# Kernel tuning notes

Hardware: AMD Instinct MI355X
Metric: run time of the kernel (lower is better)

## Reference

```python
import jax, jax.numpy as jnp
import numpy as np

ALPHA = 0.2  # LeakyReLU slope in GAT
OUT_SLOPE = 0.01  # default nn.LeakyyReLU slope for self.out
B, E, IN_DIM, HID, HEADS = 4, 2048, 32, 18, 3
DH = HID // HEADS  # per-head out dim = 6


def _leaky(x, slope):
    return jnp.where(x > 0, x, slope * x)


def _gat_head(x, adj, W, a):
    # x: [B,E,in], W: [in,dh], a: [2*dh,1]
    h = jnp.einsum('bei,id->bed', x, W)                      # [B,E,dh]
    d = h.shape[-1]
    # score[b,i,j] = leakyrelu(a . concat(h_i, h_j)) = leakyrelu(h_i.a1 + h_j.a2)
    e1 = jnp.einsum('bed,d->be', h, a[:d, 0])
    e2 = jnp.einsum('bed,d->be', h, a[d:, 0])
    score = _leaky(e1[:, :, None] + e2[:, None, :], ALPHA)   # [B,E,E]
    scores = jnp.where(adj == 1.0, score, 0.0)
    logits = jnp.where(adj > 0.0, scores, -30.0)
    att = jax.nn.softmax(logits, axis=2)                     # softmax over j
    # h_prime[b,j,d] = sum_i att[b,i,j] * h[b,i,d]  (torch sums over dim=1)
    h_prime = jnp.einsum('bij,bid->bjd', att, h)
    return jax.nn.elu(h_prime)  # concat=True -> elu


def _gat_multihead(x, adj, Ws, As):
    # Ws: [H,in,dh], As: [H,2*dh,1]
    outs = jax.vmap(lambda W, a: _gat_head(x, adj, W, a))(Ws, As)  # [H,B,E,dh]
    H, b, e, d = outs.shape
    return jnp.moveaxis(outs, 0, 2).reshape(b, e, H * d)  # concat heads last-dim


def _gcn(x, adj2d, W, b):
    return adj2d @ (x @ W) + b


def setup_inputs() -> dict:
    key = jax.random.key(0)
    ks = jax.random.split(key, 16)
    node_input = jax.random.normal(ks[0], (B, E, IN_DIM), jnp.float32)
    uv_filed = jax.random.normal(ks[1], (B, E, IN_DIM), jnp.float32)
    adj = jax.random.randint(ks[2], (B, E, E), 0, 2).astype(jnp.float32)
    s = 0.1
    Wt1 = jax.random.normal(ks[3], (HEADS, IN_DIM, DH), jnp.float32) * s
    at1 = jax.random.normal(ks[4], (HEADS, 2 * DH, 1), jnp.float32) * s
    Wt2 = jax.random.normal(ks[5], (HEADS, IN_DIM, DH), jnp.float32) * s
    at2 = jax.random.normal(ks[6], (HEADS, 2 * DH, 1), jnp.float32) * s
    Wg1 = jax.random.normal(ks[7], (HID, 16), jnp.float32) * s
    bg1 = jnp.zeros((16,), jnp.float32)
    Wg2 = jax.random.normal(ks[8], (16, 2), jnp.float32) * s
    bg2 = jnp.zeros((2,), jnp.float32)
    Wo1 = jax.random.normal(ks[9], (HID, 16), jnp.float32) * s
    bo1 = jnp.zeros((16,), jnp.float32)
    Wo2 = jax.random.normal(ks[10], (16, 2), jnp.float32) * s
    bo2 = jnp.zeros((2,), jnp.float32)
    return dict(node_input=node_input, uv_filed=uv_filed, adj=adj,
                Wt1=Wt1, at1=at1, Wt2=Wt2, at2=at2,
                Wg1=Wg1, bg1=bg1, Wg2=Wg2, bg2=bg2,
                Wo1=Wo1, bo1=bo1, Wo2=Wo2, bo2=bo2)


def reference(node_input, uv_filed, adj, Wt1, at1, Wt2, at2,
              Wg1, bg1, Wg2, bg2, Wo1, bo1, Wo2, bo2):
    h = _gat_multihead(node_input, adj, Wt1, at1)  # [B,E,18]
    o = _gat_multihead(uv_filed, adj, Wt2, at2)    # [B,E,18]
    a0 = adj[0]
    Y = jax.nn.relu(_gcn(h[0], a0, Wg1, bg1))
    O = jax.nn.relu(_gcn(o[0], a0, Wo1, bo1))
    Y = _gcn(Y, a0, Wg2, bg2)
    O = _gcn(O, a0, Wo2, bo2)
    return (jax.nn.log_softmax(Y, axis=1), _leaky(O, OUT_SLOPE))
```

## Files before the change

kernel.cpp:

```cpp
#include <hip/hip_runtime.h>
#include <hip/hip_bf16.h>


__global__ __launch_bounds__(256) void k01(
    const float* __restrict__ adj0, unsigned int* __restrict__ bm,
    const float* __restrict__ node, const float* __restrict__ uv,
    const float* __restrict__ Wt1, const float* __restrict__ at1,
    const float* __restrict__ Wt2, const float* __restrict__ at2,
    float* __restrict__ hcol, float* __restrict__ pack1, float* __restrict__ pack2) {
  int b = blockIdx.x;
  if (b < 512) {
    int lane = threadIdx.x & 63, w = threadIdx.x >> 6;
    int row = b * 4 + w;
    const float* arow = adj0 + (size_t)row * 2048;
#pragma unroll 4
    for (int it = 0; it < 32; ++it) {
      float v = arow[it * 64 + lane];
      unsigned long long mask = __ballot(v == 1.0f);
      if (lane == 0) bm[row * 64 + it * 2] = (unsigned int)mask;
      else if (lane == 32) bm[row * 64 + it * 2 + 1] = (unsigned int)(mask >> 32);
    }
    return;
  }
  __shared__ float sW[192];
  __shared__ float sA[12];
  int fb = b - 512;
  int g = fb / 24;
  int h = (fb / 8) % 3;
  int e = (fb % 8) * 256 + threadIdx.x;
  const float* W = (g ? Wt2 : Wt1) + h * 192;
  const float* A = (g ? at2 : at1) + h * 12;
  const float* x = (g ? uv : node) + e * 32;
  if (threadIdx.x < 192) sW[threadIdx.x] = W[threadIdx.x];
  if (threadIdx.x < 12) sA[threadIdx.x] = A[threadIdx.x];
  __syncthreads();
  float xv[32];
#pragma unroll
  for (int i = 0; i < 32; ++i) xv[i] = x[i];
  float hv[6];
#pragma unroll
  for (int d = 0; d < 6; ++d) hv[d] = 0.f;
#pragma unroll
  for (int i = 0; i < 32; ++i)
#pragma unroll
    for (int d = 0; d < 6; ++d) hv[d] += xv[i] * sW[i * 6 + d];
  float e1 = 0.f, e2 = 0.f;
#pragma unroll
  for (int d = 0; d < 6; ++d) {
    e1 += hv[d] * sA[d];
    e2 += hv[d] * sA[6 + d];
  }
  int c = g * 3 + h;
#pragma unroll
  for (int d = 0; d < 6; ++d) hcol[(c * 6 + d) * 2048 + e] = hv[d];
  pack1[c * 2048 + e] = e1;
  pack1[(6 + c) * 2048 + e] = __expf(e1);
  pack1[(12 + c) * 2048 + e] = __expf(0.2f * e1);
  pack2[c * 2048 + e] = e2;
  pack2[(6 + c) * 2048 + e] = __expf(e2);
  pack2[(12 + c) * 2048 + e] = __expf(0.2f * e2);
}

__global__ __launch_bounds__(384) void k2_rowsum(
    const unsigned int* __restrict__ bm, const float* __restrict__ pack1,
    const float* __restrict__ pack2, float* __restrict__ invrs) {
  int tid = threadIdx.x;
  int c = tid >> 6, lane = tid & 63;
  int i0 = blockIdx.x * 8;
  const float4* p2_4 = (const float4*)pack2;
  float e1r[8], p1r[8], q1r[8], sum[8];
#pragma unroll
  for (int r = 0; r < 8; ++r) {
    e1r[r] = pack1[c * 2048 + i0 + r];
    p1r[r] = pack1[(6 + c) * 2048 + i0 + r];
    q1r[r] = pack1[(12 + c) * 2048 + i0 + r];
    sum[r] = 0.f;
  }
  int sh = (lane & 7) * 4;
#pragma unroll
  for (int it = 0; it < 8; ++it) {
    int j4 = it * 64 + lane;
    float4 e2 = p2_4[c * 512 + j4];
    float4 p2 = p2_4[(6 + c) * 512 + j4];
    float4 q2 = p2_4[(12 + c) * 512 + j4];
    int wbase = it * 8 + (lane >> 3);
    float abx, aby, abz, abw;
#pragma unroll
    for (int r = 0; r < 8; ++r) {
      unsigned int wd = bm[(i0 + r) * 64 + wbase] >> sh;
      { float e = e1r[r] + e2.x; bool p = e > 0.f;
        abx = (p ? p1r[r] : q1r[r]) * (p ? p2.x : q2.x); }
      { float e = e1r[r] + e2.y; bool p = e > 0.f;
        aby = (p ? p1r[r] : q1r[r]) * (p ? p2.y : q2.y); }
      { float e = e1r[r] + e2.z; bool p = e > 0.f;
        abz = (p ? p1r[r] : q1r[r]) * (p ? p2.z : q2.z); }
      { float e = e1r[r] + e2.w; bool p = e > 0.f;
        abw = (p ? p1r[r] : q1r[r]) * (p ? p2.w : q2.w); }
      float s = ((wd & 1u) ? abx : 0.f) + ((wd & 2u) ? aby : 0.f) +
                ((wd & 4u) ? abz : 0.f) + ((wd & 8u) ? abw : 0.f);
      sum[r] += s;
    }
  }
#pragma unroll
  for (int r = 0; r < 8; ++r) {
#pragma unroll
    for (int off = 32; off > 0; off >>= 1) sum[r] += __shfl_down(sum[r], off);
  }
  if (lane == 0) {
#pragma unroll
    for (int r = 0; r < 8; ++r) invrs[c * 2048 + i0 + r] = 1.0f / sum[r];
  }
}

__global__ __launch_bounds__(384) void k3_hprime(
    const unsigned int* __restrict__ bm, const float* __restrict__ hcol,
    const float* __restrict__ pack1, const float* __restrict__ pack2,
    const float* __restrict__ invrs, float* __restrict__ hp_part) {
  __shared__ float4 sPack[6 * 64];
  __shared__ float sHS[6 * 64 * 8];
  __shared__ unsigned int sM[64 * 4];
  float4* sHS4 = (float4*)sHS;
  int tid = threadIdx.x;
  int c6 = tid >> 6, jl = tid & 63;
  int j0 = blockIdx.x * 128;
  int jA = j0 + jl, jB = jA + 64;
  float e2A = pack2[c6 * 2048 + jA];
  float p2A = pack2[(6 + c6) * 2048 + jA];
  float q2A = pack2[(12 + c6) * 2048 + jA];
  float e2B = pack2[c6 * 2048 + jB];
  float p2B = pack2[(6 + c6) * 2048 + jB];
  float q2B = pack2[(12 + c6) * 2048 + jB];
  float aA0 = 0.f, aA1 = 0.f, aA2 = 0.f, aA3 = 0.f, aA4 = 0.f, aA5 = 0.f;
  float aB0 = 0.f, aB1 = 0.f, aB2 = 0.f, aB3 = 0.f, aB4 = 0.f, aB5 = 0.f;
  int hi = jl >> 5;
  int shj = jl & 31;
  int ibeg = blockIdx.y * 128;
  for (int i0 = ibeg; i0 < ibeg + 128; i0 += 64) {
    __syncthreads();
    {
      int cc = c6, ii = jl;
      float e1 = pack1[cc * 2048 + i0 + ii];
      float p1 = pack1[(6 + cc) * 2048 + i0 + ii];
      float q1 = pack1[(12 + cc) * 2048 + i0 + ii];
      sPack[cc * 64 + ii] = make_float4(e1, p1, q1, 0.f);
      float iv = invrs[cc * 2048 + i0 + ii];
#pragma unroll
      for (int d = 0; d < 6; ++d)
        sHS[(cc * 64 + ii) * 8 + d] = hcol[(cc * 6 + d) * 2048 + i0 + ii] * iv;
      sHS[(cc * 64 + ii) * 8 + 6] = 0.f;
      sHS[(cc * 64 + ii) * 8 + 7] = 0.f;
    }
    if (tid < 256) sM[tid] = bm[(size_t)(i0 + (tid >> 2)) * 64 + (j0 >> 5) + (tid & 3)];
    __syncthreads();
#pragma unroll 8
    for (int ii = 0; ii < 64; ++ii) {
      float4 pk = sPack[c6 * 64 + ii];
      float4 h0 = sHS4[(c6 * 64 + ii) * 2];
      float4 h1 = sHS4[(c6 * 64 + ii) * 2 + 1];
      unsigned int wdA = sM[ii * 4 + hi];
      unsigned int wdB = sM[ii * 4 + 2 + hi];
      {
        float e = pk.x + e2A; bool p = e > 0.f;
        float ab = (p ? pk.y : pk.z) * (p ? p2A : q2A);
        float wgt = ((wdA >> shj) & 1u) ? ab : 0.f;
        aA0 += wgt * h0.x; aA1 += wgt * h0.y; aA2 += wgt * h0.z;
        aA3 += wgt * h0.w; aA4 += wgt * h1.x; aA5 += wgt * h1.y;
      }
      {
        float e = pk.x + e2B; bool p = e > 0.f;
        float ab = (p ? pk.y : pk.z) * (p ? p2B : q2B);
        float wgt = ((wdB >> shj) & 1u) ? ab : 0.f;
        aB0 += wgt * h0.x; aB1 += wgt * h0.y; aB2 += wgt * h0.z;
        aB3 += wgt * h0.w; aB4 += wgt * h1.x; aB5 += wgt * h1.y;
      }
    }
  }
  float* hp = hp_part + (size_t)blockIdx.y * 73728;
  int kb = c6 * 6;
  hp[(kb + 0) * 2048 + jA] = aA0;
  hp[(kb + 1) * 2048 + jA] = aA1;
  hp[(kb + 2) * 2048 + jA] = aA2;
  hp[(kb + 3) * 2048 + jA] = aA3;
  hp[(kb + 4) * 2048 + jA] = aA4;
  hp[(kb + 5) * 2048 + jA] = aA5;
  hp[(kb + 0) * 2048 + jB] = aB0;
  hp[(kb + 1) * 2048 + jB] = aB1;
  hp[(kb + 2) * 2048 + jB] = aB2;
  hp[(kb + 3) * 2048 + jB] = aB3;
  hp[(kb + 4) * 2048 + jB] = aB4;
  hp[(kb + 5) * 2048 + jB] = aB5;
}

__global__ __launch_bounds__(256) void k4_T(
    const float* __restrict__ hp_part, const float* __restrict__ Wg1,
    const float* __restrict__ Wo1, float* __restrict__ T) {
  __shared__ float sHP[16 * 37];
  __shared__ float sWg[288], sWo[288];
  int tid = threadIdx.x;
  int j0 = blockIdx.x * 16;
  for (int idx = tid; idx < 288; idx += 256) {
    sWg[idx] = Wg1[idx];
    sWo[idx] = Wo1[idx];
  }
  for (int idx = tid; idx < 576; idx += 256) {
    int r = idx >> 4, jl = idx & 15;
    float s = 0.f;
#pragma unroll
    for (int sp = 0; sp < 16; ++sp)
      s += hp_part[(size_t)sp * 73728 + r * 2048 + j0 + jl];
    sHP[jl * 37 + r] = s;
  }
  __syncthreads();
  int jl = tid & 15, wq = tid >> 4;
  int gat = wq >> 3;
  int c0 = (wq & 7) * 2;
  const float* Wp = gat ? sWo : sWg;
  float a0 = 0.f, a1 = 0.f;
#pragma unroll
  for (int r = 0; r < 18; ++r) {
    float x = sHP[jl * 37 + gat * 18 + r];
    float hc = x > 0.f ? x : __expf(x) - 1.f;
    a0 += hc * Wp[r * 16 + c0];
    a1 += hc * Wp[r * 16 + c0 + 1];
  }
  T[(j0 + jl) * 32 + gat * 16 + c0] = a0;
  T[(j0 + jl) * 32 + gat * 16 + c0 + 1] = a1;
}

__global__ __launch_bounds__(256) void k5_gcn1(
    const unsigned int* __restrict__ bm, const float* __restrict__ T,
    float* __restrict__ Craw_part) {
  __shared__ unsigned int sM[64 * 4];
  __shared__ float4 sT4[128 * 8];
  const float4* T4 = (const float4*)T;
  int tid = threadIdx.x;
  int rl = tid & 31, cg = tid >> 5;
  int i0 = blockIdx.x * 64;
  int k0 = blockIdx.y * 128;
  sM[tid] = bm[(size_t)(i0 + (tid >> 2)) * 64 + (k0 >> 5) + (tid & 3)];
  for (int idx = tid; idx < 1024; idx += 256) sT4[idx] = T4[k0 * 8 + idx];
  __syncthreads();
  float a0x = 0.f, a0y = 0.f, a0z = 0.f, a0w = 0.f;
  float a1x = 0.f, a1y = 0.f, a1z = 0.f, a1w = 0.f;
#pragma unroll
  for (int wi = 0; wi < 4; ++wi) {
    unsigned int wA = sM[rl * 4 + wi];
    unsigned int wB = sM[(rl + 32) * 4 + wi];
#pragma unroll 16
    for (int kb = 0; kb < 32; ++kb) {
      float4 t = sT4[(wi * 32 + kb) * 8 + cg];
      float mA = (float)((wA >> kb) & 1u);
      float mB = (float)((wB >> kb) & 1u);
      a0x += mA * t.x; a0y += mA * t.y; a0z += mA * t.z; a0w += mA * t.w;
      a1x += mB * t.x; a1y += mB * t.y; a1z += mB * t.z; a1w += mB * t.w;
    }
  }
  float* base = Craw_part + (size_t)blockIdx.y * 65536;
  *(float4*)&base[(i0 + rl) * 32 + cg * 4] = make_float4(a0x, a0y, a0z, a0w);
  *(float4*)&base[(i0 + rl + 32) * 32 + cg * 4] = make_float4(a1x, a1y, a1z, a1w);
}

__global__ __launch_bounds__(256) void k6_T2(
    const float* __restrict__ Craw_part, const float* __restrict__ bg1,
    const float* __restrict__ Wg2, const float* __restrict__ bo1,
    const float* __restrict__ Wo2, float* __restrict__ T2) {
  int tid = threadIdx.x;
  int wave = tid >> 6, lane = tid & 63;
  int j = blockIdx.x * 8 + wave * 2 + (lane >> 5);
  int cl = lane & 31;
  int gat = cl >> 4, cc = cl & 15;
  float x = 0.f;
#pragma unroll
  for (int sp = 0; sp < 16; ++sp) x += Craw_part[(size_t)sp * 65536 + j * 32 + cl];
  x += gat ? bo1[cc] : bg1[cc];
  x = x > 0.f ? x : 0.f;
  float wa = gat ? Wo2[cc * 2 + 0] : Wg2[cc * 2 + 0];
  float wb = gat ? Wo2[cc * 2 + 1] : Wg2[cc * 2 + 1];
  float pa = x * wa, pb = x * wb;
#pragma unroll
  for (int m = 8; m > 0; m >>= 1) {
    pa += __shfl_xor(pa, m);
    pb += __shfl_xor(pb, m);
  }
  if (cc == 0) {
    T2[j * 4 + gat * 2 + 0] = pa;
    T2[j * 4 + gat * 2 + 1] = pb;
  }
}

__global__ __launch_bounds__(256) void k7_final(
    const unsigned int* __restrict__ bm, const float* __restrict__ T2,
    const float* __restrict__ bg2, const float* __restrict__ bo2,
    float* __restrict__ out) {
  int tid = threadIdx.x;
  int lane = tid & 63, w = tid >> 6;
  int r = blockIdx.x * 4 + w;
  const float4* T24 = (const float4*)T2;
  float4 acc = make_float4(0.f, 0.f, 0.f, 0.f);
  int sh = lane & 31;
#pragma unroll 8
  for (int it = 0; it < 32; ++it) {
    int k = it * 64 + lane;
    unsigned int wd = bm[r * 64 + it * 2 + (lane >> 5)];
    float m = (float)((wd >> sh) & 1u);
    float4 t = T24[k];
    acc.x += m * t.x;
    acc.y += m * t.y;
    acc.z += m * t.z;
    acc.w += m * t.w;
  }
#pragma unroll
  for (int off = 32; off > 0; off >>= 1) {
    acc.x += __shfl_down(acc.x, off);
    acc.y += __shfl_down(acc.y, off);
    acc.z += __shfl_down(acc.z, off);
    acc.w += __shfl_down(acc.w, off);
  }
  if (lane == 0) {
    float y0 = acc.x + bg2[0], y1 = acc.y + bg2[1];
    float m = fmaxf(y0, y1);
    float ls = m + logf(__expf(y0 - m) + __expf(y1 - m));
    out[r * 2 + 0] = y0 - ls;
    out[r * 2 + 1] = y1 - ls;
    float o0 = acc.z + bo2[0], o1 = acc.w + bo2[1];
    out[4096 + r * 2 + 0] = o0 > 0.f ? o0 : 0.01f * o0;
    out[4096 + r * 2 + 1] = o1 > 0.f ? o1 : 0.01f * o1;
  }
}

extern "C" void kernel_launch(void* const* d_in, const int* in_sizes, int n_in,
                              void* d_out, int out_size, void* d_ws, size_t ws_size,
                              hipStream_t stream) {
  const float* node = (const float*)d_in[0];
  const float* uv = (const float*)d_in[1];
  const float* adj = (const float*)d_in[2];
  const float* Wt1 = (const float*)d_in[3];
  const float* at1 = (const float*)d_in[4];
  const float* Wt2 = (const float*)d_in[5];
  const float* at2 = (const float*)d_in[6];
  const float* Wg1 = (const float*)d_in[7];
  const float* bg1 = (const float*)d_in[8];
  const float* Wg2 = (const float*)d_in[9];
  const float* bg2 = (const float*)d_in[10];
  const float* Wo1 = (const float*)d_in[11];
  const float* bo1 = (const float*)d_in[12];
  const float* Wo2 = (const float*)d_in[13];
  const float* bo2 = (const float*)d_in[14];
  float* ws = (float*)d_ws;
  float* hcol = ws;
  float* pack1 = ws + 73728;
  float* pack2 = ws + 110592;
  float* invrs = ws + 147456;
  float* T = ws + 159744;
  float* T2 = ws + 225280;
  unsigned int* bm = (unsigned int*)(ws + 233472);
  float* hp_part = ws + 364544;
  float* Craw_part = ws + 1544192;
  float* out = (float*)d_out;

  k01<<<560, 256, 0, stream>>>(adj, bm, node, uv, Wt1, at1, Wt2, at2,
                               hcol, pack1, pack2);
  k2_rowsum<<<256, 384, 0, stream>>>(bm, pack1, pack2, invrs);
  k3_hprime<<<dim3(16, 16), 384, 0, stream>>>(bm, hcol, pack1, pack2, invrs, hp_part);
  k4_T<<<128, 256, 0, stream>>>(hp_part, Wg1, Wo1, T);
  k5_gcn1<<<dim3(32, 16), 256, 0, stream>>>(bm, T, Craw_part);
  k6_T2<<<256, 256, 0, stream>>>(Craw_part, bg1, Wg2, bo1, Wo2, T2);
  k7_final<<<512, 256, 0, stream>>>(bm, T2, bg2, bo2, out);
}
```

Before: 181.3 us.

## Transpose adjacency bitmask and rework h_prime kernel around register broadcasts

```diff
diff --git a/kernel.cpp b/kernel.cpp
--- a/kernel.cpp
+++ b/kernel.cpp
@@ -63,9 +63,24 @@
 
 __global__ __launch_bounds__(384) void k2_rowsum(
     const unsigned int* __restrict__ bm, const float* __restrict__ pack1,
-    const float* __restrict__ pack2, float* __restrict__ invrs) {
+    const float* __restrict__ pack2, const float* __restrict__ hcol,
+    unsigned int* __restrict__ bmT, float* __restrict__ hsS) {
   int tid = threadIdx.x;
   int c = tid >> 6, lane = tid & 63;
+  if (c < 4) {
+    int t = blockIdx.x * 4 + c;
+    int ti = t >> 5, tj = t & 31;
+    const unsigned int* rw = &bm[(size_t)(ti * 64 + lane) * 64 + tj * 2];
+    unsigned int rlo = rw[0], rhi = rw[1];
+    unsigned long long rowbits = ((unsigned long long)rhi << 32) | rlo;
+    unsigned int myLo = 0, myHi = 0;
+#pragma unroll
+    for (int jb = 0; jb < 64; ++jb) {
+      unsigned long long colm = __ballot((unsigned int)((rowbits >> jb) & 1ull));
+      if (jb == lane) { myLo = (unsigned int)colm; myHi = (unsigned int)(colm >> 32); }
+    }
+    *(uint2*)&bmT[(size_t)(tj * 64 + lane) * 64 + ti * 2] = make_uint2(myLo, myHi);
+  }
   int i0 = blockIdx.x * 8;
   const float4* p2_4 = (const float4*)pack2;
   float e1r[8], p1r[8], q1r[8], sum[8];
@@ -104,91 +119,88 @@
 #pragma unroll
   for (int r = 0; r < 8; ++r) {
 #pragma unroll
-    for (int off = 32; off > 0; off >>= 1) sum[r] += __shfl_down(sum[r], off);
-  }
-  if (lane == 0) {
-#pragma unroll
-    for (int r = 0; r < 8; ++r) invrs[c * 2048 + i0 + r] = 1.0f / sum[r];
-  }
-}
-
+    for (int off = 32; off > 0; off >>= 1) sum[r] += __shfl_xor(sum[r], off);
+  }
+  if (lane < 6) {
+    int row = c * 6 + lane;
+#pragma unroll
+    for (int r = 0; r < 8; ++r) {
+      float inv = 1.0f / sum[r];
+      hsS[row * 2048 + i0 + r] = hcol[row * 2048 + i0 + r] * inv;
+    }
+  }
+}
+
+#define RLF(x, l) __int_as_float(__builtin_amdgcn_readlane(__float_as_int(x), (l)))
 __global__ __launch_bounds__(384) void k3_hprime(
-    const unsigned int* __restrict__ bm, const float* __restrict__ hcol,
-    const float* __restrict__ pack1, const float* __restrict__ pack2,
-    const float* __restrict__ invrs, float* __restrict__ hp_part) {
-  __shared__ float4 sPack[6 * 64];
-  __shared__ float sHS[6 * 64 * 8];
-  __shared__ unsigned int sM[64 * 4];
-  float4* sHS4 = (float4*)sHS;
-  int tid = threadIdx.x;
-  int c6 = tid >> 6, jl = tid & 63;
-  int j0 = blockIdx.x * 128;
-  int jA = j0 + jl, jB = jA + 64;
-  float e2A = pack2[c6 * 2048 + jA];
-  float p2A = pack2[(6 + c6) * 2048 + jA];
-  float q2A = pack2[(12 + c6) * 2048 + jA];
-  float e2B = pack2[c6 * 2048 + jB];
-  float p2B = pack2[(6 + c6) * 2048 + jB];
-  float q2B = pack2[(12 + c6) * 2048 + jB];
-  float aA0 = 0.f, aA1 = 0.f, aA2 = 0.f, aA3 = 0.f, aA4 = 0.f, aA5 = 0.f;
-  float aB0 = 0.f, aB1 = 0.f, aB2 = 0.f, aB3 = 0.f, aB4 = 0.f, aB5 = 0.f;
-  int hi = jl >> 5;
-  int shj = jl & 31;
-  int ibeg = blockIdx.y * 128;
-  for (int i0 = ibeg; i0 < ibeg + 128; i0 += 64) {
-    __syncthreads();
-    {
-      int cc = c6, ii = jl;
-      float e1 = pack1[cc * 2048 + i0 + ii];
-      float p1 = pack1[(6 + cc) * 2048 + i0 + ii];
-      float q1 = pack1[(12 + cc) * 2048 + i0 + ii];
-      sPack[cc * 64 + ii] = make_float4(e1, p1, q1, 0.f);
-      float iv = invrs[cc * 2048 + i0 + ii];
-#pragma unroll
-      for (int d = 0; d < 6; ++d)
-        sHS[(cc * 64 + ii) * 8 + d] = hcol[(cc * 6 + d) * 2048 + i0 + ii] * iv;
-      sHS[(cc * 64 + ii) * 8 + 6] = 0.f;
-      sHS[(cc * 64 + ii) * 8 + 7] = 0.f;
-    }
-    if (tid < 256) sM[tid] = bm[(size_t)(i0 + (tid >> 2)) * 64 + (j0 >> 5) + (tid & 3)];
-    __syncthreads();
+    const unsigned int* __restrict__ bmT, const float* __restrict__ pack1,
+    const float* __restrict__ pack2, const float* __restrict__ hsS,
+    float* __restrict__ hp_part) {
+  int tid = threadIdx.x;
+  int c = tid >> 6, jl = tid & 63;
+  int j0 = blockIdx.x * 256;
+  int i0 = blockIdx.y * 64;
+  int il = i0 + jl;
+  float e1L = pack1[c * 2048 + il];
+  float p1L = pack1[(6 + c) * 2048 + il];
+  float q1L = pack1[(12 + c) * 2048 + il];
+  float hsL0 = hsS[(c * 6 + 0) * 2048 + il];
+  float hsL1 = hsS[(c * 6 + 1) * 2048 + il];
+  float hsL2 = hsS[(c * 6 + 2) * 2048 + il];
+  float hsL3 = hsS[(c * 6 + 3) * 2048 + il];
+  float hsL4 = hsS[(c * 6 + 4) * 2048 + il];
+  float hsL5 = hsS[(c * 6 + 5) * 2048 + il];
+  unsigned int cw0[4], cw1[4];
+#pragma unroll
+  for (int g = 0; g < 4; ++g) {
+    uint2 w = *(const uint2*)&bmT[(size_t)(j0 + g * 64 + jl) * 64 + (i0 >> 5)];
+    cw0[g] = w.x; cw1[g] = w.y;
+  }
+  float e2v[4], p2v[4], q2v[4];
+#pragma unroll
+  for (int g = 0; g < 4; ++g) {
+    int j = j0 + g * 64 + jl;
+    e2v[g] = pack2[c * 2048 + j];
+    p2v[g] = pack2[(6 + c) * 2048 + j];
+    q2v[g] = pack2[(12 + c) * 2048 + j];
+  }
+  float acc[4][6];
+#pragma unroll
+  for (int g = 0; g < 4; ++g)
+#pragma unroll
+    for (int d = 0; d < 6; ++d) acc[g][d] = 0.f;
+
+#pragma unroll
+  for (int half = 0; half < 2; ++half) {
 #pragma unroll 8
-    for (int ii = 0; ii < 64; ++ii) {
-      float4 pk = sPack[c6 * 64 + ii];
-      float4 h0 = sHS4[(c6 * 64 + ii) * 2];
-      float4 h1 = sHS4[(c6 * 64 + ii) * 2 + 1];
-      unsigned int wdA = sM[ii * 4 + hi];
-      unsigned int wdB = sM[ii * 4 + 2 + hi];
-      {
-        float e = pk.x + e2A; bool p = e > 0.f;
-        float ab = (p ? pk.y : pk.z) * (p ? p2A : q2A);
-        float wgt = ((wdA >> shj) & 1u) ? ab : 0.f;
-        aA0 += wgt * h0.x; aA1 += wgt * h0.y; aA2 += wgt * h0.z;
-        aA3 += wgt * h0.w; aA4 += wgt * h1.x; aA5 += wgt * h1.y;
+    for (int i2 = 0; i2 < 32; ++i2) {
+      int ii = half * 32 + i2;
+      float e1 = RLF(e1L, ii);
+      float p1 = RLF(p1L, ii);
+      float q1 = RLF(q1L, ii);
+      float h0 = RLF(hsL0, ii), h1 = RLF(hsL1, ii), h2 = RLF(hsL2, ii);
+      float h3 = RLF(hsL3, ii), h4 = RLF(hsL4, ii), h5 = RLF(hsL5, ii);
+#pragma unroll
+      for (int g = 0; g < 4; ++g) {
+        float e = e1 + e2v[g];
+        bool pos = e > 0.f;
+        float abp = p1 * p2v[g];
+        float abq = q1 * q2v[g];
+        float ab = pos ? abp : abq;
+        unsigned int bit = ((half ? cw1[g] : cw0[g]) >> i2) & 1u;
+        float wgt = bit ? ab : 0.f;
+        acc[g][0] += wgt * h0; acc[g][1] += wgt * h1; acc[g][2] += wgt * h2;
+        acc[g][3] += wgt * h3; acc[g][4] += wgt * h4; acc[g][5] += wgt * h5;
       }
-      {
-        float e = pk.x + e2B; bool p = e > 0.f;
-        float ab = (p ? pk.y : pk.z) * (p ? p2B : q2B);
-        float wgt = ((wdB >> shj) & 1u) ? ab : 0.f;
-        aB0 += wgt * h0.x; aB1 += wgt * h0.y; aB2 += wgt * h0.z;
-        aB3 += wgt * h0.w; aB4 += wgt * h1.x; aB5 += wgt * h1.y;
-      }
     }
   }
   float* hp = hp_part + (size_t)blockIdx.y * 73728;
-  int kb = c6 * 6;
-  hp[(kb + 0) * 2048 + jA] = aA0;
-  hp[(kb + 1) * 2048 + jA] = aA1;
-  hp[(kb + 2) * 2048 + jA] = aA2;
-  hp[(kb + 3) * 2048 + jA] = aA3;
-  hp[(kb + 4) * 2048 + jA] = aA4;
-  hp[(kb + 5) * 2048 + jA] = aA5;
-  hp[(kb + 0) * 2048 + jB] = aB0;
-  hp[(kb + 1) * 2048 + jB] = aB1;
-  hp[(kb + 2) * 2048 + jB] = aB2;
-  hp[(kb + 3) * 2048 + jB] = aB3;
-  hp[(kb + 4) * 2048 + jB] = aB4;
-  hp[(kb + 5) * 2048 + jB] = aB5;
+#pragma unroll
+  for (int g = 0; g < 4; ++g) {
+    int j = j0 + g * 64 + jl;
+#pragma unroll
+    for (int d = 0; d < 6; ++d) hp[(c * 6 + d) * 2048 + j] = acc[g][d];
+  }
 }
 
 __global__ __launch_bounds__(256) void k4_T(
@@ -206,7 +218,7 @@
     int r = idx >> 4, jl = idx & 15;
     float s = 0.f;
 #pragma unroll
-    for (int sp = 0; sp < 16; ++sp)
+    for (int sp = 0; sp < 32; ++sp)
       s += hp_part[(size_t)sp * 73728 + r * 2048 + j0 + jl];
     sHP[jl * 37 + r] = s;
   }
@@ -350,18 +362,19 @@
   float* hcol = ws;
   float* pack1 = ws + 73728;
   float* pack2 = ws + 110592;
-  float* invrs = ws + 147456;
-  float* T = ws + 159744;
-  float* T2 = ws + 225280;
-  unsigned int* bm = (unsigned int*)(ws + 233472);
-  float* hp_part = ws + 364544;
-  float* Craw_part = ws + 1544192;
+  float* hsS = ws + 147456;
+  float* T = ws + 221184;
+  float* T2 = ws + 286720;
+  unsigned int* bm = (unsigned int*)(ws + 294912);
+  unsigned int* bmT = (unsigned int*)(ws + 425984);
+  float* hp_part = ws + 557056;
+  float* Craw_part = ws + 2916352;
   float* out = (float*)d_out;
 
   k01<<<560, 256, 0, stream>>>(adj, bm, node, uv, Wt1, at1, Wt2, at2,
                                hcol, pack1, pack2);
-  k2_rowsum<<<256, 384, 0, stream>>>(bm, pack1, pack2, invrs);
-  k3_hprime<<<dim3(16, 16), 384, 0, stream>>>(bm, hcol, pack1, pack2, invrs, hp_part);
+  k2_rowsum<<<256, 384, 0, stream>>>(bm, pack1, pack2, hcol, bmT, hsS);
+  k3_hprime<<<dim3(8, 32), 384, 0, stream>>>(bmT, pack1, pack2, hsS, hp_part);
   k4_T<<<128, 256, 0, stream>>>(hp_part, Wg1, Wo1, T);
   k5_gcn1<<<dim3(32, 16), 256, 0, stream>>>(bm, T, Craw_part);
   k6_T2<<<256, 256, 0, stream>>>(Craw_part, bg1, Wg2, bo1, Wo2, T2);
```

Result: slower. 185.0 us (+2.0%).
